# Kernel optimization log

Measured on AMD Instinct MI355X. Metric: run time of the kernel, lower is better.

The kernel has to match this reference:

```python
import jax, jax.numpy as jnp
import numpy as np

LN_EPS = 1e-5

def _ln(x):
    # haiku LayerNorm([-1], create_scale=False, create_offset=False)
    mu = x.mean(axis=-1, keepdims=True)
    var = x.var(axis=-1, keepdims=True)
    return (x - mu) * jax.lax.rsqrt(var + LN_EPS)

def setup_inputs() -> dict:
    key = jax.random.key(0)
    ks = jax.random.split(key, 10)
    N, L, P = 512, 256, 64
    inp = {
        "local": jax.random.normal(ks[0], (N, L), jnp.float32),
        "pair": jax.random.normal(ks[1], (N, N, P), jnp.float32),
        "mask": jax.random.randint(ks[2], (N,), 0, 2, jnp.int32),
        "W_pair_gate": jax.random.normal(ks[3], (P, 2 * P), jnp.float32) / np.sqrt(P),
        "W_pair_value": jax.random.normal(ks[4], (P, 2 * P), jnp.float32) / np.sqrt(P),
        "W_left_gate": jax.random.normal(ks[5], (L, 2 * P), jnp.float32) / np.sqrt(L),
        "W_left_value": jax.random.normal(ks[6], (L, 2 * P), jnp.float32) / np.sqrt(L),
        "W_right_gate": jax.random.normal(ks[7], (L, 2 * P), jnp.float32) / np.sqrt(L),
        "W_right_value": jax.random.normal(ks[8], (L, 2 * P), jnp.float32) / np.sqrt(L),
        "W_out": jax.random.normal(ks[9], (3 * P, P), jnp.float32) / np.sqrt(3 * P),
    }
    return inp

def reference(local, pair, mask, W_pair_gate, W_pair_value, W_left_gate,
              W_left_value, W_right_gate, W_right_value, W_out):
    maskb = mask.astype(bool)
    pair_mask = maskb[:, None] & maskb[None, :]                  # (N, N)
    l = _ln(local)                                               # (N, L)
    p = _ln(pair)                                                # (N, N, P)
    pair_gate = p @ W_pair_gate                                  # (N, N, 2P)
    pair_value = p @ W_pair_value                                # (N, N, 2P)
    # left: broadcast local over axis 0/1, gelu-gate, mask, reduce over j
    left_gate = jax.nn.gelu((l @ W_left_gate)[:, None] + pair_gate)
    left_value = (l @ W_left_value)[None, :] + pair_value
    left = jnp.where(pair_mask[..., None], left_gate * left_value, 0).sum(axis=1)  # (N, 2P)
    right_gate = jax.nn.gelu((l @ W_right_gate)[None, :] + pair_gate)
    right_value = (l @ W_right_value)[:, None] + pair_value
    right = jnp.where(pair_mask[..., None], right_gate * right_value, 0).sum(axis=0)  # (N, 2P)
    paired_pseudo_local = _ln(left[:, None] + right[None, :])    # (N, N, 2P)
    pair_hidden = jnp.concatenate((p, paired_pseudo_local), axis=-1)  # (N, N, 3P)
    return pair_hidden @ W_out                                   # (N, N, P)
```

## Files before the change

### kernel.cpp

```cpp
#include <hip/hip_runtime.h>
#include <math.h>

#define LN_EPS 1e-5f


typedef __bf16 bf16x8 __attribute__((ext_vector_type(8)));
typedef float f32x16 __attribute__((ext_vector_type(16)));

__device__ __forceinline__ float gelu_f(float x) {
    float x2 = x * x;
    float e = __builtin_amdgcn_exp2f(x * fmaf(0.10294423f, x2, 2.3022079f));
    float r = __builtin_amdgcn_rcpf(e + 1.0f);
    return fmaf(-x, r, x);
}

__global__ __launch_bounds__(256) void kA(
    const float* __restrict__ loc,
    const float* __restrict__ Wlg, const float* __restrict__ Wlv,
    const float* __restrict__ Wrg, const float* __restrict__ Wrv,
    float* __restrict__ proj, const int* __restrict__ mask,
    int* __restrict__ act, float* __restrict__ left, float* __restrict__ right) {
    const int t = threadIdx.x;
    if (blockIdx.x == 64) {
        if (blockIdx.y == 1) {
            float4 z = {0.f, 0.f, 0.f, 0.f};
            for (int idx = t; idx < 16384; idx += 256) ((float4*)left)[idx] = z;
        } else if (blockIdx.y == 2) {
            float4 z = {0.f, 0.f, 0.f, 0.f};
            for (int idx = t; idx < 16384; idx += 256) ((float4*)right)[idx] = z;
        } else if (blockIdx.y == 0) {
            __shared__ int cnt_sh[8];
            const int lane = t & 63, wv = t >> 6;
            int msave[2];
            unsigned long long bsave[2];
#pragma unroll
            for (int ch = 0; ch < 2; ++ch) {
                int m = (mask[ch * 256 + t] != 0);
                unsigned long long b = __ballot(m);
                if (lane == 0) cnt_sh[ch * 4 + wv] = __popcll(b);
                msave[ch] = m;
                bsave[ch] = b;
            }
            __syncthreads();
#pragma unroll
            for (int ch = 0; ch < 2; ++ch) {
                int base = 0;
                for (int u = 0; u < ch * 4 + wv; ++u) base += cnt_sh[u];
                int pos = base + __popcll(bsave[ch] & ((1ull << lane) - 1ull));
                if (msave[ch]) act[1 + pos] = ch * 256 + t;
            }
            if (t == 0) {
                int ctot = 0;
                for (int u = 0; u < 8; ++u) ctot += cnt_sh[u];
                act[0] = ctot;
            }
        }
        return;
    }
    __shared__ float ln_sh[8][260];
    __shared__ float red_sh[128][9];
    const int i0 = blockIdx.x * 8;
    const int mat = blockIdx.y;
    const float* __restrict__ W = (mat == 0) ? Wlg : (mat == 1) ? Wlv
                                 : (mat == 2) ? Wrg : Wrv;
    {
        int row = t >> 5, l32 = t & 31;
        const float4* src = (const float4*)(loc + (i0 + row) * 256);
        float4 v0 = src[l32 * 2];
        float4 v1 = src[l32 * 2 + 1];
        float s = (v0.x + v0.y) + (v0.z + v0.w) + (v1.x + v1.y) + (v1.z + v1.w);
        float ss = v0.x * v0.x + v0.y * v0.y + v0.z * v0.z + v0.w * v0.w +
                   v1.x * v1.x + v1.y * v1.y + v1.z * v1.z + v1.w * v1.w;
#pragma unroll
        for (int off = 1; off < 32; off <<= 1) {
            s += __shfl_xor(s, off);
            ss += __shfl_xor(ss, off);
        }
        float mu = s * (1.f / 256.f);
        float rs = rsqrtf(ss * (1.f / 256.f) - mu * mu + LN_EPS);
        float4 o0, o1;
        o0.x = (v0.x - mu) * rs; o0.y = (v0.y - mu) * rs;
        o0.z = (v0.z - mu) * rs; o0.w = (v0.w - mu) * rs;
        o1.x = (v1.x - mu) * rs; o1.y = (v1.y - mu) * rs;
        o1.z = (v1.z - mu) * rs; o1.w = (v1.w - mu) * rs;
        *(float4*)&ln_sh[row][l32 * 8] = o0;
        *(float4*)&ln_sh[row][l32 * 8 + 4] = o1;
    }
    __syncthreads();

    const int n = t & 127;
    const int kh = t >> 7;
    float acc[8] = {0.f, 0.f, 0.f, 0.f, 0.f, 0.f, 0.f, 0.f};
#pragma unroll 2
    for (int c = 0; c < 32; ++c) {
        const int kc = kh * 128 + c * 4;
        float w0 = W[(kc + 0) * 128 + n];
        float w1 = W[(kc + 1) * 128 + n];
        float w2 = W[(kc + 2) * 128 + n];
        float w3 = W[(kc + 3) * 128 + n];
#pragma unroll
        for (int r = 0; r < 8; ++r) {
            float4 l4 = *(const float4*)&ln_sh[r][kc];
            acc[r] += l4.x * w0 + l4.y * w1 + l4.z * w2 + l4.w * w3;
        }
    }
    if (kh == 1) {
#pragma unroll
        for (int r = 0; r < 8; ++r) red_sh[n][r] = acc[r];
    }
    __syncthreads();
    if (kh == 0) {
#pragma unroll
        for (int r = 0; r < 8; ++r)
            proj[mat * 65536 + (i0 + r) * 128 + n] = acc[r] + red_sh[n][r];
    }
}

#define KB_TI 8
__global__ __launch_bounds__(256) void kB(
    const float* __restrict__ pair, const int* __restrict__ act,
    const float* __restrict__ Wg, const float* __restrict__ Wv,
    const float* __restrict__ lg, const float* __restrict__ lv,
    const float* __restrict__ rg, const float* __restrict__ rv,
    float* __restrict__ left, float* __restrict__ right) {
    __shared__ __bf16 A_sh[2][32][72];
    __shared__ int ji_sh[32];
    __shared__ int ii_sh[KB_TI];

    const int cnt = act[0];
    const int j0 = blockIdx.x * 32;
    const int ibase = blockIdx.y * KB_TI;
    if (j0 >= cnt || ibase >= cnt) return;
    const int nact = min(KB_TI, cnt - ibase);

    const int t = threadIdx.x;
    const int lane = t & 63;
    const int w = t >> 6;
    const int c = lane & 31;
    const int half = lane >> 5;
    const int n = w * 32 + c;

    if (t < 32) ji_sh[t] = act[1 + min(j0 + t, cnt - 1)];
    if (t >= 64 && t < 64 + KB_TI) ii_sh[t - 64] = act[1 + min(ibase + (t - 64), cnt - 1)];
    __syncthreads();

    bf16x8 bg[4], bv[4];
#pragma unroll
    for (int kt = 0; kt < 4; ++kt) {
        bf16x8 vg, vv;
#pragma unroll
        for (int e = 0; e < 8; ++e) {
            int kr = kt * 16 + half * 8 + e;
            vg[e] = (__bf16)Wg[kr * 128 + n];
            vv[e] = (__bf16)Wv[kr * 128 + n];
        }
        bg[kt] = vg; bv[kt] = vv;
    }

    float lvr[16], rgr[16];
    unsigned jmask = 0;
#pragma unroll
    for (int r = 0; r < 16; ++r) {
        int m = 4 * half + (r & 3) + 8 * (r >> 2);
        int j = ji_sh[m];
        lvr[r] = lv[j * 128 + n];
        rgr[r] = rg[j * 128 + n];
        if (j0 + m < cnt) jmask |= (1u << r);
    }

    const int srow = t >> 3;
    const int kseg = (t & 7) * 8;
    float4 p0, p1;
    float plg, prv;
    {
        int iF = ii_sh[0];
        const float* src = pair + ((size_t)iF * 512 + ji_sh[srow]) * 64 + kseg;
        p0 = *(const float4*)src;
        p1 = *(const float4*)(src + 4);
        plg = lg[iF * 128 + n];
        prv = rv[iF * 128 + n];
    }

    auto lnwrite = [&](int buf) {
        float s = (p0.x + p0.y) + (p0.z + p0.w) + (p1.x + p1.y) + (p1.z + p1.w);
        float ss = p0.x * p0.x + p0.y * p0.y + p0.z * p0.z + p0.w * p0.w +
                   p1.x * p1.x + p1.y * p1.y + p1.z * p1.z + p1.w * p1.w;
        s += __shfl_xor(s, 1); ss += __shfl_xor(ss, 1);
        s += __shfl_xor(s, 2); ss += __shfl_xor(ss, 2);
        s += __shfl_xor(s, 4); ss += __shfl_xor(ss, 4);
        float mu = s * (1.f / 64.f);
        float rs = rsqrtf(ss * (1.f / 64.f) - mu * mu + LN_EPS);
        bf16x8 o;
        o[0] = (__bf16)((p0.x - mu) * rs); o[1] = (__bf16)((p0.y - mu) * rs);
        o[2] = (__bf16)((p0.z - mu) * rs); o[3] = (__bf16)((p0.w - mu) * rs);
        o[4] = (__bf16)((p1.x - mu) * rs); o[5] = (__bf16)((p1.y - mu) * rs);
        o[6] = (__bf16)((p1.z - mu) * rs); o[7] = (__bf16)((p1.w - mu) * rs);
        *(bf16x8*)&A_sh[buf][srow][kseg] = o;
    };
    lnwrite(0);
    __syncthreads();

    float racc[16];
#pragma unroll
    for (int r = 0; r < 16; ++r) racc[r] = 0.f;

    for (int ii = 0; ii < nact; ++ii) {
        const int i = ii_sh[ii];
        const float lgi = plg;
        const float rvi = prv;
        if (ii + 1 < nact) {
            int iF = ii_sh[ii + 1];
            const float* src = pair + ((size_t)iF * 512 + ji_sh[srow]) * 64 + kseg;
            p0 = *(const float4*)src;
            p1 = *(const float4*)(src + 4);
            plg = lg[iF * 128 + n];
            prv = rv[iF * 128 + n];
        }

        f32x16 ag = {}; f32x16 av = {};
#pragma unroll
        for (int kt = 0; kt < 4; ++kt) {
            bf16x8 af = *(const bf16x8*)&A_sh[ii & 1][c][kt * 16 + half * 8];
            ag = __builtin_amdgcn_mfma_f32_32x32x16_bf16(af, bg[kt], ag, 0, 0, 0);
            av = __builtin_amdgcn_mfma_f32_32x32x16_bf16(af, bv[kt], av, 0, 0, 0);
        }

        float lsum = 0.f;
#pragma unroll
        for (int r = 0; r < 16; ++r) {
            float pg = ag[r], pv = av[r];
            float lres = gelu_f(lgi + pg) * (lvr[r] + pv);
            float rres = gelu_f(rgr[r] + pg) * (rvi + pv);
            lsum += ((jmask >> r) & 1) ? lres : 0.f;
            racc[r] += rres;
        }
        float tot = lsum + __shfl_xor(lsum, 32);
        if (lane < 32) atomicAdd(&left[i * 128 + n], tot);

        if (ii + 1 < nact) lnwrite((ii + 1) & 1);
        __syncthreads();
    }

#pragma unroll
    for (int r = 0; r < 16; ++r) {
        if ((jmask >> r) & 1) {
            int m = 4 * half + (r & 3) + 8 * (r >> 2);
            atomicAdd(&right[ji_sh[m] * 128 + n], racc[r]);
        }
    }
}

__global__ __launch_bounds__(256) void kD(
    const float* __restrict__ left, const float* __restrict__ right,
    const float* __restrict__ W_out,
    float* __restrict__ Aw, float* __restrict__ Bw,
    float* __restrict__ sums, float* __restrict__ cs, float* __restrict__ C) {
    const int bx = blockIdx.x;
    const int t = threadIdx.x;
    if (bx < 256) {
        __shared__ float l_sh[32][68];
        __shared__ float r_sh[32][68];
        const int tx = t & 15, ty = t >> 4;
        const int i0 = (bx & 15) * 32, j0 = (bx >> 4) * 32;
        float acc00 = 0.f, acc01 = 0.f, acc10 = 0.f, acc11 = 0.f;
        for (int kc = 0; kc < 128; kc += 64) {
            __syncthreads();
#pragma unroll
            for (int u = 0; u < 2; ++u) {
                int fi = t + u * 256;
                int row = fi >> 4, kq = (fi & 15) * 4;
                float4 lv4 = *(const float4*)(left + (i0 + row) * 128 + kc + kq);
                float4 rv4 = *(const float4*)(right + (j0 + row) * 128 + kc + kq);
                *(float4*)&l_sh[row][kq] = lv4;
                *(float4*)&r_sh[row][kq] = rv4;
            }
            __syncthreads();
#pragma unroll 8
            for (int k = 0; k < 64; ++k) {
                float l0 = l_sh[ty * 2 + 0][k], l1 = l_sh[ty * 2 + 1][k];
                float r0 = r_sh[tx * 2 + 0][k], r1 = r_sh[tx * 2 + 1][k];
                acc00 += l0 * r0; acc01 += l0 * r1;
                acc10 += l1 * r0; acc11 += l1 * r1;
            }
        }
        C[(size_t)(i0 + ty * 2 + 0) * 512 + j0 + tx * 2 + 0] = acc00;
        C[(size_t)(i0 + ty * 2 + 0) * 512 + j0 + tx * 2 + 1] = acc01;
        C[(size_t)(i0 + ty * 2 + 1) * 512 + j0 + tx * 2 + 0] = acc10;
        C[(size_t)(i0 + ty * 2 + 1) * 512 + j0 + tx * 2 + 1] = acc11;
    } else {
        const int id = bx - 256;
        const int which = id >> 8;
        const int sub = t >> 7;
        const int tt = t & 127;
        const int r = (id & 255) * 2 + sub;
        const float* src = which ? right : left;
        __shared__ float row_sh[2][128];
        __shared__ float red[2][4];
        float v = src[r * 128 + tt];
        row_sh[sub][tt] = v;
        float s = v, ss = v * v;
#pragma unroll
        for (int off = 1; off < 64; off <<= 1) {
            s += __shfl_xor(s, off);
            ss += __shfl_xor(ss, off);
        }
        int wid = tt >> 6, lane = tt & 63;
        if (lane == 0) { red[sub][wid * 2] = s; red[sub][wid * 2 + 1] = ss; }
        __syncthreads();
        if (tt == 0) {
            sums[which * 1024 + r] = red[sub][0] + red[sub][2];
            sums[which * 1024 + 512 + r] = red[sub][1] + red[sub][3];
        }
        if (tt < 64) {
            float a = 0.f;
            const float* W2 = W_out + 64 * 64;
#pragma unroll 8
            for (int m = 0; m < 128; ++m) a += row_sh[sub][m] * W2[m * 64 + tt];
            (which ? Bw : Aw)[r * 64 + tt] = a;
        }
        if (id == 0 && t < 64) {
            float c0 = 0.f, c1 = 0.f;
            for (int k = 0; k < 64; ++k) c0 += W_out[k * 64 + t];
            for (int m = 0; m < 128; ++m) c1 += W_out[(64 + m) * 64 + t];
            cs[t] = c0;
            cs[64 + t] = c1;
        }
    }
}

__global__ __launch_bounds__(256) void kC(
    const float* __restrict__ pair, const float* __restrict__ Wout,
    const float* __restrict__ Aw, const float* __restrict__ Bw,
    const float* __restrict__ Cw, const float* __restrict__ sums,
    const float* __restrict__ cs, float* __restrict__ out) {
    const int t = threadIdx.x;
    const int lane = t & 63;
    const int w = t >> 6;
    const int c = lane & 31;
    const int half = lane >> 5;
    const int i0 = blockIdx.x * 4;
    const int j0 = blockIdx.y * 64;
    const int mt = w & 1;
    const int nt = w >> 1;
    const int n = nt * 32 + c;
    const int jrow = j0 + mt * 32 + c;

    const float* __restrict__ abase = pair + ((size_t)i0 * 512 + jrow) * 64 + half * 8;

    float4 va[8], vb[8];
#pragma unroll
    for (int kt = 0; kt < 4; ++kt) {
        va[2 * kt] = *(const float4*)(abase + kt * 16);
        va[2 * kt + 1] = *(const float4*)(abase + kt * 16 + 4);
    }

    bf16x8 bo[4];
#pragma unroll
    for (int kt = 0; kt < 4; ++kt) {
        bf16x8 bb;
#pragma unroll
        for (int e = 0; e < 8; ++e)
            bb[e] = (__bf16)Wout[(kt * 16 + half * 8 + e) * 64 + n];
        bo[kt] = bb;
    }
    float Bv[16];
#pragma unroll
    for (int r = 0; r < 16; ++r) {
        int jp = j0 + mt * 32 + 4 * half + (r & 3) + 8 * (r >> 2);
        Bv[r] = Bw[jp * 64 + n];
    }
    const float cs1n = cs[64 + n];

    auto body = [&](float4 (&cur)[8], float4 (&nxt)[8], int ii) {
        if (ii < 3) {
            const float* src = abase + (size_t)(ii + 1) * 512 * 64;
#pragma unroll
            for (int kt = 0; kt < 4; ++kt) {
                nxt[2 * kt] = *(const float4*)(src + kt * 16);
                nxt[2 * kt + 1] = *(const float4*)(src + kt * 16 + 4);
            }
        }
        const int i = i0 + ii;
        float Cv[16];
#pragma unroll
        for (int r = 0; r < 16; ++r) {
            int jp = j0 + mt * 32 + 4 * half + (r & 3) + 8 * (r >> 2);
            Cv[r] = Cw[(size_t)i * 512 + jp];
        }
        const float A_in = Aw[i * 64 + n];
        const float sumLi = sums[i], ssLi = sums[512 + i];

        float s = 0.f, ss = 0.f;
#pragma unroll
        for (int u = 0; u < 8; ++u) {
            s += (cur[u].x + cur[u].y) + (cur[u].z + cur[u].w);
            ss += cur[u].x * cur[u].x + cur[u].y * cur[u].y +
                  cur[u].z * cur[u].z + cur[u].w * cur[u].w;
        }
        s += __shfl_xor(s, 32);
        ss += __shfl_xor(ss, 32);
        float mu = s * (1.f / 64.f);
        float rs = rsqrtf(ss * (1.f / 64.f) - mu * mu + LN_EPS);

        f32x16 acc = {};
#pragma unroll
        for (int kt = 0; kt < 4; ++kt) {
            bf16x8 af;
#pragma unroll
            for (int u = 0; u < 2; ++u) {
                float4 vv = cur[2 * kt + u];
                af[u * 4 + 0] = (__bf16)((vv.x - mu) * rs);
                af[u * 4 + 1] = (__bf16)((vv.y - mu) * rs);
                af[u * 4 + 2] = (__bf16)((vv.z - mu) * rs);
                af[u * 4 + 3] = (__bf16)((vv.w - mu) * rs);
            }
            acc = __builtin_amdgcn_mfma_f32_32x32x16_bf16(af, bo[kt], acc, 0, 0, 0);
        }

#pragma unroll
        for (int r = 0; r < 16; ++r) {
            int jp = j0 + mt * 32 + 4 * half + (r & 3) + 8 * (r >> 2);
            float sR = sums[1024 + jp], ssR = sums[1536 + jp];
            float mu_s = (sumLi + sR) * (1.f / 128.f);
            float var_s = fmaf(-mu_s, mu_s, (ssLi + 2.f * Cv[r] + ssR) * (1.f / 128.f));
            float rs_s = rsqrtf(var_s + LN_EPS);
            out[((size_t)i * 512 + jp) * 64 + n] =
                fmaf(rs_s, (A_in + Bv[r]) - mu_s * cs1n, acc[r]);
        }
    };
    body(va, vb, 0);
    body(vb, va, 1);
    body(va, vb, 2);
    body(vb, va, 3);
}

extern "C" void kernel_launch(void* const* d_in, const int* in_sizes, int n_in,
                              void* d_out, int out_size, void* d_ws, size_t ws_size,
                              hipStream_t stream) {
    const float* loc  = (const float*)d_in[0];
    const float* pair = (const float*)d_in[1];
    const int*   mask = (const int*)d_in[2];
    const float* Wpg  = (const float*)d_in[3];
    const float* Wpv  = (const float*)d_in[4];
    const float* Wlg  = (const float*)d_in[5];
    const float* Wlv  = (const float*)d_in[6];
    const float* Wrg  = (const float*)d_in[7];
    const float* Wrv  = (const float*)d_in[8];
    const float* Wout = (const float*)d_in[9];
    float* out = (float*)d_out;
    float* ws = (float*)d_ws;

    float* proj  = ws;
    float* left  = ws + 262144;
    float* right = ws + 327680;
    float* Aw    = ws + 393216;
    float* Bw    = ws + 425984;
    float* Cw    = ws + 458752;
    float* sums  = ws + 720896;
    float* cs    = ws + 722944;
    int*   act   = (int*)(ws + 723072);

    kA<<<dim3(65, 4), 256, 0, stream>>>(loc, Wlg, Wlv, Wrg, Wrv, proj,
                                        mask, act, left, right);
    kB<<<dim3(16, 64), 256, 0, stream>>>(pair, act, Wpg, Wpv,
                                         proj, proj + 65536, proj + 131072,
                                         proj + 196608, left, right);
    kD<<<768, 256, 0, stream>>>(left, right, Wout, Aw, Bw, sums, cs, Cw);
    kC<<<dim3(128, 8), 256, 0, stream>>>(pair, Wout, Aw, Bw, Cw, sums, cs, out);
}
```

Measured before the change: 191.3 us.

## Precompute per-pair layernorm scale in kD and halve kB i-tile

```diff
diff --git a/kernel.cpp b/kernel.cpp
--- a/kernel.cpp
+++ b/kernel.cpp
@@ -116,7 +116,7 @@
     }
 }
 
-#define KB_TI 8
+#define KB_TI 4
 __global__ __launch_bounds__(256) void kB(
     const float* __restrict__ pair, const int* __restrict__ act,
     const float* __restrict__ Wg, const float* __restrict__ Wv,
@@ -254,7 +254,8 @@
     const float* __restrict__ left, const float* __restrict__ right,
     const float* __restrict__ W_out,
     float* __restrict__ Aw, float* __restrict__ Bw,
-    float* __restrict__ sums, float* __restrict__ cs, float* __restrict__ C) {
+    float* __restrict__ rsArr, float* __restrict__ rmArr,
+    float* __restrict__ cs) {
     const int bx = blockIdx.x;
     const int t = threadIdx.x;
     if (bx < 256) {
@@ -263,6 +264,8 @@
         const int tx = t & 15, ty = t >> 4;
         const int i0 = (bx & 15) * 32, j0 = (bx >> 4) * 32;
         float acc00 = 0.f, acc01 = 0.f, acc10 = 0.f, acc11 = 0.f;
+        float sL0 = 0.f, ssL0 = 0.f, sL1 = 0.f, ssL1 = 0.f;
+        float sR0 = 0.f, ssR0 = 0.f, sR1 = 0.f, ssR1 = 0.f;
         for (int kc = 0; kc < 128; kc += 64) {
             __syncthreads();
 #pragma unroll
@@ -281,12 +284,30 @@
                 float r0 = r_sh[tx * 2 + 0][k], r1 = r_sh[tx * 2 + 1][k];
                 acc00 += l0 * r0; acc01 += l0 * r1;
                 acc10 += l1 * r0; acc11 += l1 * r1;
-            }
-        }
-        C[(size_t)(i0 + ty * 2 + 0) * 512 + j0 + tx * 2 + 0] = acc00;
-        C[(size_t)(i0 + ty * 2 + 0) * 512 + j0 + tx * 2 + 1] = acc01;
-        C[(size_t)(i0 + ty * 2 + 1) * 512 + j0 + tx * 2 + 0] = acc10;
-        C[(size_t)(i0 + ty * 2 + 1) * 512 + j0 + tx * 2 + 1] = acc11;
+                sL0 += l0; ssL0 += l0 * l0;
+                sL1 += l1; ssL1 += l1 * l1;
+                sR0 += r0; ssR0 += r0 * r0;
+                sR1 += r1; ssR1 += r1 * r1;
+            }
+        }
+        {
+            float sLa[2] = {sL0, sL1}, ssLa[2] = {ssL0, ssL1};
+            float sRb[2] = {sR0, sR1}, ssRb[2] = {ssR0, ssR1};
+            float accv[2][2] = {{acc00, acc01}, {acc10, acc11}};
+#pragma unroll
+            for (int a = 0; a < 2; ++a) {
+#pragma unroll
+                for (int b = 0; b < 2; ++b) {
+                    float mu = (sLa[a] + sRb[b]) * (1.f / 128.f);
+                    float var = fmaf(-mu, mu,
+                                     (ssLa[a] + 2.f * accv[a][b] + ssRb[b]) * (1.f / 128.f));
+                    float rs = rsqrtf(var + LN_EPS);
+                    size_t idx = (size_t)(i0 + ty * 2 + a) * 512 + (j0 + tx * 2 + b);
+                    rsArr[idx] = rs;
+                    rmArr[idx] = rs * mu;
+                }
+            }
+        }
     } else {
         const int id = bx - 256;
         const int which = id >> 8;
@@ -295,22 +316,8 @@
         const int r = (id & 255) * 2 + sub;
         const float* src = which ? right : left;
         __shared__ float row_sh[2][128];
-        __shared__ float red[2][4];
-        float v = src[r * 128 + tt];
-        row_sh[sub][tt] = v;
-        float s = v, ss = v * v;
-#pragma unroll
-        for (int off = 1; off < 64; off <<= 1) {
-            s += __shfl_xor(s, off);
-            ss += __shfl_xor(ss, off);
-        }
-        int wid = tt >> 6, lane = tt & 63;
-        if (lane == 0) { red[sub][wid * 2] = s; red[sub][wid * 2 + 1] = ss; }
+        row_sh[sub][tt] = src[r * 128 + tt];
         __syncthreads();
-        if (tt == 0) {
-            sums[which * 1024 + r] = red[sub][0] + red[sub][2];
-            sums[which * 1024 + 512 + r] = red[sub][1] + red[sub][3];
-        }
         if (tt < 64) {
             float a = 0.f;
             const float* W2 = W_out + 64 * 64;
@@ -331,7 +338,7 @@
 __global__ __launch_bounds__(256) void kC(
     const float* __restrict__ pair, const float* __restrict__ Wout,
     const float* __restrict__ Aw, const float* __restrict__ Bw,
-    const float* __restrict__ Cw, const float* __restrict__ sums,
+    const float* __restrict__ rsArr, const float* __restrict__ rmArr,
     const float* __restrict__ cs, float* __restrict__ out) {
     const int t = threadIdx.x;
     const int lane = t & 63;
@@ -381,14 +388,7 @@
             }
         }
         const int i = i0 + ii;
-        float Cv[16];
-#pragma unroll
-        for (int r = 0; r < 16; ++r) {
-            int jp = j0 + mt * 32 + 4 * half + (r & 3) + 8 * (r >> 2);
-            Cv[r] = Cw[(size_t)i * 512 + jp];
-        }
         const float A_in = Aw[i * 64 + n];
-        const float sumLi = sums[i], ssLi = sums[512 + i];
 
         float s = 0.f, ss = 0.f;
 #pragma unroll
@@ -420,12 +420,11 @@
 #pragma unroll
         for (int r = 0; r < 16; ++r) {
             int jp = j0 + mt * 32 + 4 * half + (r & 3) + 8 * (r >> 2);
-            float sR = sums[1024 + jp], ssR = sums[1536 + jp];
-            float mu_s = (sumLi + sR) * (1.f / 128.f);
-            float var_s = fmaf(-mu_s, mu_s, (ssLi + 2.f * Cv[r] + ssR) * (1.f / 128.f));
-            float rs_s = rsqrtf(var_s + LN_EPS);
-            out[((size_t)i * 512 + jp) * 64 + n] =
-                fmaf(rs_s, (A_in + Bv[r]) - mu_s * cs1n, acc[r]);
+            size_t idx = (size_t)i * 512 + jp;
+            float rsv = rsArr[idx];
+            float rmv = rmArr[idx];
+            out[idx * 64 + n] =
+                fmaf(rsv, A_in + Bv[r], fmaf(-rmv, cs1n, acc[r]));
         }
     };
     body(va, vb, 0);
@@ -455,16 +454,16 @@
     float* right = ws + 327680;
     float* Aw    = ws + 393216;
     float* Bw    = ws + 425984;
-    float* Cw    = ws + 458752;
-    float* sums  = ws + 720896;
+    float* rsA   = ws + 458752;
+    float* rmA   = ws;
     float* cs    = ws + 722944;
     int*   act   = (int*)(ws + 723072);
 
     kA<<<dim3(65, 4), 256, 0, stream>>>(loc, Wlg, Wlv, Wrg, Wrv, proj,
                                         mask, act, left, right);
-    kB<<<dim3(16, 64), 256, 0, stream>>>(pair, act, Wpg, Wpv,
-                                         proj, proj + 65536, proj + 131072,
-                                         proj + 196608, left, right);
-    kD<<<768, 256, 0, stream>>>(left, right, Wout, Aw, Bw, sums, cs, Cw);
-    kC<<<dim3(128, 8), 256, 0, stream>>>(pair, Wout, Aw, Bw, Cw, sums, cs, out);
-}
+    kB<<<dim3(16, 128), 256, 0, stream>>>(pair, act, Wpg, Wpv,
+                                          proj, proj + 65536, proj + 131072,
+                                          proj + 196608, left, right);
+    kD<<<768, 256, 0, stream>>>(left, right, Wout, Aw, Bw, rsA, rmA, cs);
+    kC<<<dim3(128, 8), 256, 0, stream>>>(pair, Wout, Aw, Bw, rsA, rmA, cs, out);
+}
```

New measurement: 190.9 us. Within noise of the previous version (-0.3%).
